# Performance work log

Measured on AMD Instinct MI355X. Metric: run time of the kernel, lower is better.

The kernel has to match this reference:

```python
import jax, jax.numpy as jnp
import numpy as np
import math

D_K = 8  # = n_wires; one input value encoded per wire


def setup_inputs() -> dict:
    key = jax.random.key(0)
    k1, k2, k3, k4 = jax.random.split(key, 4)
    B, S, E = 4, 2048, 1024
    x = jax.random.normal(k1, (B, S, E), dtype=jnp.float32)
    theta = jax.random.normal(k2, (D_K,), dtype=jnp.float32)  # shared RX params (one ModuleList reused per head)
    W = jax.random.normal(k3, (E, E), dtype=jnp.float32) * (1.0 / math.sqrt(E))
    b = jax.random.normal(k4, (E,), dtype=jnp.float32) * 0.01
    return {"x": x, "theta": theta, "W": W, "b": b}


def reference(x, theta, W, b):
    B, S, E = x.shape
    dk = theta.shape[0]
    H = E // dk
    # Quantum circuit collapse: RX(x_i) then RX(theta_i) on |0>, measure PauliZ
    # on each wire of a product state -> <Z_i> = cos(x_i + theta_i).
    proj = x.reshape(B, S, H, dk)
    q_out = jnp.cos(proj + theta)  # theta broadcast over (B,S,H)
    # NOTE: faithful to original — attention is over the HEAD axis: (B,S,H,H)
    attn = jnp.einsum('bshd,bsgd->bshg', q_out, q_out) / math.sqrt(dk)
    attn = jax.nn.softmax(attn, axis=-1)  # dropout is identity at inference
    out = jnp.einsum('bshg,bsgd->bshd', attn, q_out)  # (B,S,H,dk)
    # faithful transpose(1,2).contiguous().view(B,S,E) reinterleave
    out = jnp.transpose(out, (0, 2, 1, 3)).reshape(B, S, E)
    return out @ W.T + b
```

## Files before the change

kernel.cpp:

```cpp
#include <hip/hip_runtime.h>
#include <hip/hip_bf16.h>
#include <stdint.h>

typedef __attribute__((ext_vector_type(8))) short bf16x8;
typedef __attribute__((ext_vector_type(4))) float f32x4;
typedef __attribute__((ext_vector_type(16))) float f32x16;
typedef __attribute__((ext_vector_type(2))) unsigned int uint32x2;
typedef __attribute__((address_space(3))) void lds_t;
typedef __attribute__((address_space(1))) void glb_t;

#define B_ 4
#define S_ 2048
#define E_ 1024
#define M_ (B_*S_)
#define QTS 152
#define NPOS 4

static __device__ __forceinline__ ushort f2bf(float f) {
  uint32_t u = __float_as_uint(f);
  u += 0x7fffu + ((u >> 16) & 1u);
  return (ushort)(u >> 16);
}

static __device__ __forceinline__ uint32_t pk_bf16(float lo, float hi) {
  uint32_t r;
  asm("v_cvt_pk_bf16_f32 %0, %1, %2" : "=v"(r) : "v"(lo), "v"(hi));
  return r;
}
static __device__ __forceinline__ float fexp2(float x) {
  float r;
  asm("v_exp_f32 %0, %1" : "=v"(r) : "v"(x));
  return r;
}

static __device__ __forceinline__ void half_zip(uint32_t a, uint32_t b, bool convA,
                                                uint32_t& X, uint32_t& Y) {
  if (convA) {
    uint32x2 r = __builtin_amdgcn_permlane32_swap(b, a, false, false);
    Y = r[0]; X = r[1];
  } else {
    uint32x2 r = __builtin_amdgcn_permlane32_swap(a, b, false, false);
    X = r[0]; Y = r[1];
  }
}

__global__ __launch_bounds__(256) void qattn(const float* __restrict__ x,
                                             const float* __restrict__ theta,
                                             ushort* __restrict__ outr) {
  const int wave = threadIdx.x >> 6;
  const int lane = threadIdx.x & 63;
  const int l31 = lane & 31, hw = lane >> 5;

  const int bid = blockIdx.x;
  const int base = ((bid & 7) * 256 + (bid >> 3)) * NPOS;

  __shared__ __align__(16) ushort qL[2][129 * 8];
  __shared__ __align__(16) ushort qT[2][16 * QTS];

  uint32x2 pr = __builtin_amdgcn_permlane32_swap((uint32_t)lane, (uint32_t)(lane + 1000),
                                                 false, false);
  const bool convA = (__builtin_amdgcn_readfirstlane((int)pr[0]) >= 1000);

  auto gen = [&](int bs_g, int sel) {
    ushort* qpg = qL[sel];
    ushort* qtg = qT[sel];
    const int h  = 32 * wave + (lane >> 1);
    const int dh = (lane & 1) * 4;
    const float4 xv = *(const float4*)(x + (size_t)bs_g * E_ + h * 8 + dh);
    float q[4];
    q[0] = __cosf(xv.x + theta[dh + 0]);
    q[1] = __cosf(xv.y + theta[dh + 1]);
    q[2] = __cosf(xv.z + theta[dh + 2]);
    q[3] = __cosf(xv.w + theta[dh + 3]);

    const float QS = 0.71419165f;
    uint2 pw;
    pw.x = pk_bf16(q[0] * QS, q[1] * QS);
    pw.y = pk_bf16(q[2] * QS, q[3] * QS);
    *(uint2*)(qpg + h * 8 + dh) = pw;

    #pragma unroll
    for (int j = 0; j < 4; ++j)
      qtg[(dh + j) * QTS + h] = f2bf(q[j]);
    #pragma unroll
    for (int j = 0; j < 4; ++j)
      qtg[(8 + dh + j) * QTS + h] = (j == 0) ? (ushort)0x3F80u : (ushort)0u;

    if (lane == 0) *(uint4*)(qpg + 128 * 8) = make_uint4(0, 0, 0, 0);
  };

  gen(base, 0);
  __syncthreads();
  __builtin_amdgcn_sched_barrier(0);

  #pragma unroll
  for (int i = 0; i < NPOS; ++i) {
    const int sel = i & 1;
    if (i + 1 < NPOS) gen(base + i + 1, sel ^ 1);

    const ushort* qp = qL[sel];
    const ushort* qt = qT[sel];
    const int bs = base + i;
    const int b = bs >> 11, s = bs & 2047;

    bf16x8 qtf[8];
    const bf16x8 zf = {};
    #pragma unroll
    for (int ks = 0; ks < 8; ++ks) {
      bf16x8 f = *(const bf16x8*)(qt + (l31 & 15) * QTS + ks * 16 + hw * 8);
      qtf[ks] = (l31 < 16) ? f : zf;
    }

    const int hi = wave;
    const int brow = (lane < 32) ? (hi * 32 + l31) : 128;
    const bf16x8 bq = *(const bf16x8*)(qp + brow * 8);

    f32x16 oacc = {};

    #pragma unroll
    for (int gj = 0; gj < 4; ++gj) {
      const int arow = (lane < 32) ? (gj * 32 + l31) : 128;
      const bf16x8 aq = *(const bf16x8*)(qp + arow * 8);
      f32x16 sc = {};
      sc = __builtin_amdgcn_mfma_f32_32x32x16_bf16(aq, bq, sc, 0, 0, 0);
      float pv[16];
      #pragma unroll
      for (int k = 0; k < 16; ++k) pv[k] = fexp2(sc[k]);
      #pragma unroll
      for (int sl = 0; sl < 2; ++sl) {
        const int pb = sl * 8;
        const uint32_t u = pk_bf16(pv[pb+0], pv[pb+1]);
        const uint32_t v = pk_bf16(pv[pb+2], pv[pb+3]);
        const uint32_t w = pk_bf16(pv[pb+4], pv[pb+5]);
        const uint32_t z = pk_bf16(pv[pb+6], pv[pb+7]);
        uint32_t f0, f1, f2, f3;
        half_zip(u, w, convA, f0, f2);
        half_zip(v, z, convA, f1, f3);
        uint32_t fr[4] = {f0, f1, f2, f3};
        oacc = __builtin_amdgcn_mfma_f32_32x32x16_bf16(qtf[gj*2 + sl], *(const bf16x8*)fr,
                                                       oacc, 0, 0, 0);
      }
    }

    const int scol = s & 127, srow = s >> 7;
    const float inv = __builtin_amdgcn_rcpf(oacc[4]);
    const uint32_t o01 = pk_bf16(oacc[0] * inv, oacc[1] * inv);
    const uint32_t o23 = pk_bf16(oacc[2] * inv, oacc[3] * inv);
    const int h = hi * 32 + l31;
    const size_t row = (size_t)(b * 2048 + h * 16 + srow);
    *(uint2*)(outr + row * E_ + scol * 8 + hw * 4) = make_uint2(o01, o23);

    __syncthreads();
    __builtin_amdgcn_sched_barrier(0);
  }
}

__global__ __launch_bounds__(256) void wconv(const float* __restrict__ W,
                                             ushort* __restrict__ Wb) {
  const int i = blockIdx.x * 256 + threadIdx.x;
  const float4 v = ((const float4*)W)[i];
  ushort4 o;
  o.x = f2bf(v.x); o.y = f2bf(v.y); o.z = f2bf(v.z); o.w = f2bf(v.w);
  ((ushort4*)Wb)[i] = o;
}

__global__ __launch_bounds__(256) void gemm_bt(const ushort* __restrict__ A,
                                               const ushort* __restrict__ Bw,
                                               const float* __restrict__ bias,
                                               float* __restrict__ C) {
  __shared__ __align__(16) ushort As[128 * 32];
  __shared__ __align__(16) ushort Bs[128 * 32];

  const int t = threadIdx.x;
  const int lane = t & 63;
  const int wavei = t >> 6;
  const int wr = wavei >> 1, wc = wavei & 1;
  const int lhi = lane >> 4, llo = lane & 15;
  const size_t ar0 = (size_t)blockIdx.x * 128;
  const size_t br0 = (size_t)blockIdx.y * 128;

  const int c0 = t, c1 = t + 256;
  const int r0 = c0 >> 2, kp0 = (c0 & 3) * 8;
  const int r1 = c1 >> 2, kp1 = (c1 & 3) * 8;

  f32x4 acc[4][4] = {};

  for (int k0 = 0; k0 < E_; k0 += 32) {
    __builtin_amdgcn_global_load_lds((const glb_t*)(A  + (ar0 + r0) * E_ + k0 + kp0),
                                     (lds_t*)(As + c0 * 8), 16, 0, 0);
    __builtin_amdgcn_global_load_lds((const glb_t*)(A  + (ar0 + r1) * E_ + k0 + kp1),
                                     (lds_t*)(As + c1 * 8), 16, 0, 0);
    __builtin_amdgcn_global_load_lds((const glb_t*)(Bw + (br0 + r0) * E_ + k0 + kp0),
                                     (lds_t*)(Bs + c0 * 8), 16, 0, 0);
    __builtin_amdgcn_global_load_lds((const glb_t*)(Bw + (br0 + r1) * E_ + k0 + kp1),
                                     (lds_t*)(Bs + c1 * 8), 16, 0, 0);
    __syncthreads();

    bf16x8 af[4], bfr[4];
    #pragma unroll
    for (int i = 0; i < 4; ++i)
      af[i] = *(const bf16x8*)(As + (wr * 64 + i * 16 + llo) * 32 + lhi * 8);
    #pragma unroll
    for (int j = 0; j < 4; ++j)
      bfr[j] = *(const bf16x8*)(Bs + (wc * 64 + j * 16 + llo) * 32 + lhi * 8);

    #pragma unroll
    for (int i = 0; i < 4; ++i)
      #pragma unroll
      for (int j = 0; j < 4; ++j)
        acc[i][j] = __builtin_amdgcn_mfma_f32_16x16x32_bf16(af[i], bfr[j], acc[i][j], 0, 0, 0);

    __syncthreads();
  }

  #pragma unroll
  for (int j = 0; j < 4; ++j) {
    const int n = (int)br0 + wc * 64 + j * 16 + llo;
    const float bj = bias[n];
    #pragma unroll
    for (int i = 0; i < 4; ++i) {
      const int mb = (int)ar0 + wr * 64 + i * 16 + lhi * 4;
      #pragma unroll
      for (int r = 0; r < 4; ++r) {
        C[(size_t)(mb + r) * E_ + n] = acc[i][j][r] + bj;
      }
    }
  }
}

extern "C" void kernel_launch(void* const* d_in, const int* in_sizes, int n_in,
                              void* d_out, int out_size, void* d_ws, size_t ws_size,
                              hipStream_t stream) {
  const float* x     = (const float*)d_in[0];
  const float* theta = (const float*)d_in[1];
  const float* W     = (const float*)d_in[2];
  const float* bias  = (const float*)d_in[3];
  float* out = (float*)d_out;

  ushort* outr = (ushort*)d_ws;
  ushort* Wb   = (ushort*)((char*)d_ws + (size_t)M_ * E_ * 2);

  qattn<<<M_ / NPOS, 256, 0, stream>>>(x, theta, outr);
  wconv<<<(E_ * E_) / (256 * 4), 256, 0, stream>>>(W, Wb);
  dim3 g(M_ / 128, E_ / 128);
  gemm_bt<<<g, 256, 0, stream>>>(outr, Wb, bias, out);
}
```

Before: 75.25 us.

## Process two positions per block with upfront generation, drop per-step barriers

The attention kernel now handles two (b,s) positions per block instead of four. It generates both positions' LDS tiles up front and drops the double-buffered in-loop generation and per-iteration __syncthreads. Fragment loads for the transposed Q tile move inside the head-group loop to lower register pressure, and the A-operand loads are hoisted ahead of the loop. This doubles the grid size to give more parallelism and removes sync stalls, at the cost of losing overlap between generation and compute inside a block.

```diff
diff --git a/kernel.cpp b/kernel.cpp
--- a/kernel.cpp
+++ b/kernel.cpp
@@ -14,7 +14,7 @@
 #define E_ 1024
 #define M_ (B_*S_)
 #define QTS 152
-#define NPOS 4
+#define PPB 2
 
 static __device__ __forceinline__ ushort f2bf(float f) {
   uint32_t u = __float_as_uint(f);
@@ -52,10 +52,10 @@
   const int l31 = lane & 31, hw = lane >> 5;
 
   const int bid = blockIdx.x;
-  const int base = ((bid & 7) * 256 + (bid >> 3)) * NPOS;
-
-  __shared__ __align__(16) ushort qL[2][129 * 8];
-  __shared__ __align__(16) ushort qT[2][16 * QTS];
+  const int pair = (bid & 7) * 512 + (bid >> 3);
+
+  __shared__ __align__(16) ushort qL[PPB][129 * 8];
+  __shared__ __align__(16) ushort qT[PPB][16 * QTS];
 
   uint32x2 pr = __builtin_amdgcn_permlane32_swap((uint32_t)lane, (uint32_t)(lane + 1000),
                                                  false, false);
@@ -89,29 +89,27 @@
     if (lane == 0) *(uint4*)(qpg + 128 * 8) = make_uint4(0, 0, 0, 0);
   };
 
-  gen(base, 0);
+  gen(pair * PPB + 0, 0);
+  gen(pair * PPB + 1, 1);
   __syncthreads();
   __builtin_amdgcn_sched_barrier(0);
 
+  const int hi = wave;
+  const bf16x8 zf = {};
+
   #pragma unroll
-  for (int i = 0; i < NPOS; ++i) {
-    const int sel = i & 1;
-    if (i + 1 < NPOS) gen(base + i + 1, sel ^ 1);
-
-    const ushort* qp = qL[sel];
-    const ushort* qt = qT[sel];
-    const int bs = base + i;
+  for (int pp = 0; pp < PPB; ++pp) {
+    const ushort* qp = qL[pp];
+    const ushort* qt = qT[pp];
+    const int bs = pair * PPB + pp;
     const int b = bs >> 11, s = bs & 2047;
 
-    bf16x8 qtf[8];
-    const bf16x8 zf = {};
-    #pragma unroll
-    for (int ks = 0; ks < 8; ++ks) {
-      bf16x8 f = *(const bf16x8*)(qt + (l31 & 15) * QTS + ks * 16 + hw * 8);
-      qtf[ks] = (l31 < 16) ? f : zf;
+    bf16x8 aqv[4];
+    #pragma unroll
+    for (int gj = 0; gj < 4; ++gj) {
+      const int arow = (lane < 32) ? (gj * 32 + l31) : 128;
+      aqv[gj] = *(const bf16x8*)(qp + arow * 8);
     }
-
-    const int hi = wave;
     const int brow = (lane < 32) ? (hi * 32 + l31) : 128;
     const bf16x8 bq = *(const bf16x8*)(qp + brow * 8);
 
@@ -119,10 +117,12 @@
 
     #pragma unroll
     for (int gj = 0; gj < 4; ++gj) {
-      const int arow = (lane < 32) ? (gj * 32 + l31) : 128;
-      const bf16x8 aq = *(const bf16x8*)(qp + arow * 8);
       f32x16 sc = {};
-      sc = __builtin_amdgcn_mfma_f32_32x32x16_bf16(aq, bq, sc, 0, 0, 0);
+      sc = __builtin_amdgcn_mfma_f32_32x32x16_bf16(aqv[gj], bq, sc, 0, 0, 0);
+      bf16x8 fA = *(const bf16x8*)(qt + (l31 & 15) * QTS + (gj * 2 + 0) * 16 + hw * 8);
+      bf16x8 fB = *(const bf16x8*)(qt + (l31 & 15) * QTS + (gj * 2 + 1) * 16 + hw * 8);
+      fA = (l31 < 16) ? fA : zf;
+      fB = (l31 < 16) ? fB : zf;
       float pv[16];
       #pragma unroll
       for (int k = 0; k < 16; ++k) pv[k] = fexp2(sc[k]);
@@ -137,7 +137,8 @@
         half_zip(u, w, convA, f0, f2);
         half_zip(v, z, convA, f1, f3);
         uint32_t fr[4] = {f0, f1, f2, f3};
-        oacc = __builtin_amdgcn_mfma_f32_32x32x16_bf16(qtf[gj*2 + sl], *(const bf16x8*)fr,
+        oacc = __builtin_amdgcn_mfma_f32_32x32x16_bf16((sl == 0) ? fA : fB,
+                                                       *(const bf16x8*)fr,
                                                        oacc, 0, 0, 0);
       }
     }
@@ -149,9 +150,6 @@
     const int h = hi * 32 + l31;
     const size_t row = (size_t)(b * 2048 + h * 16 + srow);
     *(uint2*)(outr + row * E_ + scol * 8 + hw * 4) = make_uint2(o01, o23);
-
-    __syncthreads();
-    __builtin_amdgcn_sched_barrier(0);
   }
 }
 
@@ -240,7 +238,7 @@
   ushort* outr = (ushort*)d_ws;
   ushort* Wb   = (ushort*)((char*)d_ws + (size_t)M_ * E_ * 2);
 
-  qattn<<<M_ / NPOS, 256, 0, stream>>>(x, theta, outr);
+  qattn<<<M_ / PPB, 256, 0, stream>>>(x, theta, outr);
   wconv<<<(E_ * E_) / (256 * 4), 256, 0, stream>>>(W, Wb);
   dim3 g(M_ / 128, E_ / 128);
   gemm_bt<<<g, 256, 0, stream>>>(outr, Wb, bias, out);
```

New measurement: 70.46 us. 1.07x faster.
